# Kernel tuning notes

Measured on AMD Instinct MI355X. Metric: run time of the kernel, lower is better.

## Reference

```python
import jax, jax.numpy as jnp
import numpy as np

P_DROP = 0.1
NTYPES = 8
DROP_KEY = jax.random.key(42)


def _dropout(h, i):
    # deterministic training-mode dropout, mask fixed by layer index
    keep = jax.random.bernoulli(jax.random.fold_in(DROP_KEY, i), 1.0 - P_DROP, h.shape)
    return jnp.where(keep, h / (1.0 - P_DROP), 0.0).astype(h.dtype)


def _func_conv(h, src, dst, types, convW, convb, act):
    # gather src features along edges, mean-aggregate onto dst nodes,
    # then apply a per-gate-type linear transform.
    n_out = types.shape[0]
    msg = h[src]                                                  # [E, d]
    agg = jax.ops.segment_sum(msg, dst, num_segments=n_out)       # [n_out, d]
    deg = jax.ops.segment_sum(jnp.ones((src.shape[0],), h.dtype), dst,
                              num_segments=n_out)
    agg = agg / jnp.maximum(deg, 1.0)[:, None]
    out = jnp.zeros((n_out, convW.shape[2]), h.dtype)
    for t in range(convW.shape[0]):                                # ntypes is small & fixed
        mask = (types == t).astype(h.dtype)[:, None]
        out = out + (agg * mask) @ convW[t]
    out = out + convb[types]
    return jax.nn.relu(out) if act else out


def setup_inputs() -> dict:
    key = jax.random.key(0)
    ks = jax.random.split(key, 16)
    N0, N1, N2, N3 = 400_000, 200_000, 100_000, 50_000
    E0, E1, E2 = 1_600_000, 800_000, 400_000
    d, dout = 128, 64
    inp = {
        "features": jax.random.normal(ks[0], (N0, d), jnp.float32),
        "src0": jax.random.randint(ks[1], (E0,), 0, N0),
        "dst0": jax.random.randint(ks[2], (E0,), 0, N1),
        "types1": jax.random.randint(ks[3], (N1,), 0, NTYPES),
        "src1": jax.random.randint(ks[4], (E1,), 0, N1),
        "dst1": jax.random.randint(ks[5], (E1,), 0, N2),
        "types2": jax.random.randint(ks[6], (N2,), 0, NTYPES),
        "src2": jax.random.randint(ks[7], (E2,), 0, N2),
        "dst2": jax.random.randint(ks[8], (E2,), 0, N3),
        "types3": jax.random.randint(ks[9], (N3,), 0, NTYPES),
        # learned params
        "convW": jax.random.normal(ks[10], (NTYPES, d, d), jnp.float32) / np.sqrt(d),
        "convb": jnp.zeros((NTYPES, d), jnp.float32),
        "fcW": jax.random.normal(ks[11], (d, dout), jnp.float32) / np.sqrt(d),
        "fcb": jnp.zeros((dout,), jnp.float32),
    }
    return inp


def reference(features, src0, dst0, types1, src1, dst1, types2,
              src2, dst2, types3, convW, convb, fcW, fcb):
    blocks = [(src0, dst0, types1), (src1, dst1, types2), (src2, dst2, types3)]
    depth = len(blocks)
    h = features
    for i, (s, dst, t) in enumerate(blocks):
        if i != 0:
            h = _dropout(h, i)
        h = _func_conv(h, s, dst, t, convW, convb, act=(i != depth - 1))
    h = h @ fcW + fcb   # hidden_dim != out_dim -> fc_out applied
    return h            # squeeze(1) is a no-op for out_dim > 1
```

## Files before the change

### kernel.cpp

```cpp
#include <hip/hip_runtime.h>
#include <cstdint>
#include <cstddef>

__host__ __device__ inline void tf2x32(uint32_t k0, uint32_t k1,
                                       uint32_t x0, uint32_t x1,
                                       uint32_t* o0, uint32_t* o1)
{
    uint32_t ks2 = k0 ^ k1 ^ 0x1BD11BDAu;
    x0 += k0; x1 += k1;
#define TF_R(r) do { x0 += x1; x1 = (x1 << (r)) | (x1 >> (32 - (r))); x1 ^= x0; } while (0)
    TF_R(13); TF_R(15); TF_R(26); TF_R(6);
    x0 += k1;  x1 += ks2 + 1u;
    TF_R(17); TF_R(29); TF_R(16); TF_R(24);
    x0 += ks2; x1 += k0 + 2u;
    TF_R(13); TF_R(15); TF_R(26); TF_R(6);
    x0 += k0;  x1 += k1 + 3u;
    TF_R(17); TF_R(29); TF_R(16); TF_R(24);
    x0 += k1;  x1 += ks2 + 4u;
    TF_R(13); TF_R(15); TF_R(26); TF_R(6);
    x0 += ks2; x1 += k0 + 5u;
#undef TF_R
    *o0 = x0; *o1 = x1;
}

__device__ inline float drop_scale(uint32_t fk0, uint32_t fk1, uint32_t idx)
{
    uint32_t o0, o1;
    tf2x32(fk0, fk1, 0u, idx, &o0, &o1);
    uint32_t bits = o0 ^ o1;
    float u = __uint_as_float((bits >> 9) | 0x3f800000u) - 1.0f;
    return (u < 0.9f) ? (1.0f / 0.9f) : 0.0f;
}

__device__ inline ushort bf16_rn(float f)
{
    uint32_t u = __float_as_uint(f);
    u += 0x7fffu + ((u >> 16) & 1u);
    return (ushort)(u >> 16);
}
__device__ inline float bf16_f(ushort h) { return __uint_as_float(((uint32_t)h) << 16); }
__device__ inline uint32_t pack2bf(float a, float b)
{
    return (uint32_t)bf16_rn(a) | ((uint32_t)bf16_rn(b) << 16);
}
__device__ inline float bflo(uint32_t u) { return __uint_as_float(u << 16); }
__device__ inline float bfhi(uint32_t u) { return __uint_as_float(u & 0xffff0000u); }

typedef __attribute__((ext_vector_type(8))) short bf16x8;
typedef __attribute__((ext_vector_type(4))) float f32x4;

__global__ __launch_bounds__(256) void fcvt_kernel(
    const float4* __restrict__ in, uint2* __restrict__ out, long long n4)
{
    long long stride = (long long)gridDim.x * 256;
    for (long long i = blockIdx.x * 256LL + threadIdx.x; i < n4; i += stride) {
        float4 v = in[i];
        out[i] = make_uint2(pack2bf(v.x, v.y), pack2bf(v.z, v.w));
    }
}

__global__ __launch_bounds__(256) void prep_all_kernel(
    const float* __restrict__ convW, const float* __restrict__ convb,
    const float* __restrict__ fcW, const float* __restrict__ fcb,
    ushort* __restrict__ WThi, ushort* __restrict__ WTlo,
    ushort* __restrict__ WfThi, ushort* __restrict__ WfTlo,
    float* __restrict__ bfb)
{
    __shared__ float F[128 * 64];
    int t = blockIdx.x, tid = threadIdx.x;
    #pragma unroll
    for (int it = 0; it < 8; ++it) {
        int idx4 = (it * 256 + tid) * 4;
        *(float4*)&F[idx4] = *(const float4*)&fcW[idx4];
    }
    __syncthreads();

    {
        const float* S = convW + (size_t)t * 16384;
        ushort* DH = WThi + (size_t)t * 16384;
        ushort* DL = WTlo + (size_t)t * 16384;
        for (int idx = tid; idx < 16384; idx += 256) {
            int k = idx >> 7, c = idx & 127;
            float v = S[idx];
            ushort hi = bf16_rn(v);
            ushort lo = bf16_rn(v - bf16_f(hi));
            int pos = c * 128 + ((((k >> 3) ^ (c & 15)) << 3) | (k & 7));
            DH[pos] = hi; DL[pos] = lo;
        }
    }

    {
        int r = tid >> 1, cb = (tid & 1) * 32;
        const float* Wrow = convW + (size_t)t * 16384 + (size_t)r * 128;
        float acc[32];
        #pragma unroll
        for (int c = 0; c < 32; ++c) acc[c] = 0.f;
        for (int k = 0; k < 128; ++k) {
            float w = Wrow[k];
            #pragma unroll
            for (int c = 0; c < 32; ++c) acc[c] += w * F[k * 64 + cb + c];
        }
        ushort* FH = WfThi + (size_t)t * 8192;
        ushort* FL = WfTlo + (size_t)t * 8192;
        int swzr = (r & 7);
        #pragma unroll
        for (int c = 0; c < 32; ++c) {
            int col = cb + c;
            float v = acc[c];
            ushort hi = bf16_rn(v);
            ushort lo = bf16_rn(v - bf16_f(hi));
            int pos = col * 128 + ((((r >> 3) ^ (col & 15)) << 3) | swzr);
            FH[pos] = hi; FL[pos] = lo;
        }
    }

    if (tid < 64) {
        float a = fcb[tid];
        const float* bt = convb + (size_t)t * 128;
        for (int k = 0; k < 128; ++k) a += bt[k] * F[k * 64 + tid];
        bfb[(size_t)t * 64 + tid] = a;
    }
}

#define EPB 4096

__global__ __launch_bounds__(256) void hist_all_kernel(
    const int* __restrict__ d0, const int* __restrict__ d1, const int* __restrict__ d2,
    const int* __restrict__ t1, const int* __restrict__ t2, const int* __restrict__ t3,
    int E0, int E1, int E2, int N1, int N2, int N3,
    int nb0, int nb1, int nb2, int nblk0, int nblk1, int nblk2,
    uint32_t* __restrict__ tot, uint32_t* __restrict__ tcnt)
{
    int L = blockIdx.y;
    int tid = threadIdx.x;
    if (L < 3) {
        const int* dst = L == 0 ? d0 : (L == 1 ? d1 : d2);
        int E  = L == 0 ? E0 : (L == 1 ? E1 : E2);
        int NB = L == 0 ? nb0 : (L == 1 ? nb1 : nb2);
        int nblk = L == 0 ? nblk0 : (L == 1 ? nblk1 : nblk2);
        int gO = L == 0 ? 0 : (L == 1 ? nb0 : nb0 + nb1);
        if ((int)blockIdx.x >= nblk) return;
        __shared__ uint32_t lh[256];
        lh[tid] = 0;
        __syncthreads();
        int base = blockIdx.x * EPB;
        for (int i = tid; i < EPB; i += 256) {
            int e = base + i;
            if (e < E) atomicAdd(&lh[((uint32_t)dst[e]) >> 10], 1u);
        }
        __syncthreads();
        if (tid < NB && lh[tid]) atomicAdd(&tot[gO + tid], lh[tid]);
    } else {
        int totalN = N1 + N2 + N3;
        if ((int)blockIdx.x * 256 >= totalN) return;
        __shared__ uint32_t lh[24];
        if (tid < 24) lh[tid] = 0;
        __syncthreads();
        int i = blockIdx.x * 256 + tid;
        if (i < N1) atomicAdd(&lh[t1[i]], 1u);
        else if (i < N1 + N2) atomicAdd(&lh[8 + t2[i - N1]], 1u);
        else if (i < totalN) atomicAdd(&lh[16 + t3[i - N1 - N2]], 1u);
        __syncthreads();
        if (tid < 24 && lh[tid]) atomicAdd(&tcnt[tid], lh[tid]);
    }
}

__global__ __launch_bounds__(512) void scan_all_kernel(
    const uint32_t* __restrict__ tot, uint32_t* __restrict__ bo,
    uint32_t* __restrict__ bcur, uint32_t* __restrict__ rowptr3,
    const uint32_t* __restrict__ tcnt, int* __restrict__ boff,
    uint32_t* __restrict__ tcur, int* __restrict__ order3,
    int nb0, int nb1, int nb2, int N1, int N2, int N3,
    int r1, int r2, int no1p, int no2p)
{
    __shared__ uint32_t bol[348];
    __shared__ int pB[27];
    __shared__ int cnts[24];
    int t = threadIdx.x;
    int TB = nb0 + nb1 + nb2;
    if (t < 3) {
        int nb = t == 0 ? nb0 : (t == 1 ? nb1 : nb2);
        int g0 = t == 0 ? 0 : (t == 1 ? nb0 : nb0 + nb1);
        int gi0 = g0 + t;
        uint32_t run = 0;
        for (int i = 0; i < nb; ++i) { bol[gi0 + i] = run; run += tot[g0 + i]; }
        bol[gi0 + nb] = run;
        int rp = t == 0 ? 0 : (t == 1 ? r1 : r2);
        int N = t == 0 ? N1 : (t == 1 ? N2 : N3);
        rowptr3[rp + N] = run;
    }
    if (t == 3) {
        for (int L = 0; L < 3; ++L) {
            int a = 0;
            for (int ty = 0; ty < 8; ++ty) {
                pB[L * 9 + ty] = a;
                int c = (int)tcnt[L * 8 + ty];
                cnts[L * 8 + ty] = c;
                tcur[L * 8 + ty] = (uint32_t)a;
                a += (c + 127) & ~127;
            }
            pB[L * 9 + 8] = a;
        }
    }
    __syncthreads();
    for (int i = t; i < TB + 3; i += 512) bo[i] = bol[i];
    if (t < TB) {
        int layer = t < nb0 ? 0 : (t < nb0 + nb1 ? 1 : 2);
        bcur[t] = bol[t + layer];
    }
    if (t < 27) boff[t] = pB[t];
    if (t < 24) {
        int L = t >> 3, ty = t & 7;
        int noff = L == 0 ? 0 : (L == 1 ? no1p : no2p);
        int s = pB[L * 9 + ty] + cnts[t];
        int e2 = pB[L * 9 + ty + 1];
        for (int k = s; k < e2; ++k) order3[noff + k] = -1;
    }
}

__global__ __launch_bounds__(256) void scatter_all_kernel(
    const int* __restrict__ s0, const int* __restrict__ d0,
    const int* __restrict__ s1, const int* __restrict__ d1,
    const int* __restrict__ s2, const int* __restrict__ d2,
    const int* __restrict__ t1, const int* __restrict__ t2, const int* __restrict__ t3,
    int E0, int E1, int E2, int N1, int N2, int N3,
    int nb0, int nb1, int nb2, int nblk0, int nblk1, int nblk2,
    uint32_t* __restrict__ bcur, uint32_t* __restrict__ pairs,
    uint32_t* __restrict__ tcur, int* __restrict__ order3, int no1p, int no2p)
{
    int L = blockIdx.y;
    int tid = threadIdx.x;
    if (L < 3) {
        const int* src = L == 0 ? s0 : (L == 1 ? s1 : s2);
        const int* dst = L == 0 ? d0 : (L == 1 ? d1 : d2);
        int E  = L == 0 ? E0 : (L == 1 ? E1 : E2);
        int NB = L == 0 ? nb0 : (L == 1 ? nb1 : nb2);
        int nblk = L == 0 ? nblk0 : (L == 1 ? nblk1 : nblk2);
        int gO = L == 0 ? 0 : (L == 1 ? nb0 : nb0 + nb1);
        uint32_t* pr = pairs + (L == 0 ? 0 : (L == 1 ? E0 : E0 + E1));
        if ((int)blockIdx.x >= nblk) return;

        __shared__ uint32_t lh[256], lbase[256], rank[256];
        lh[tid] = 0; rank[tid] = 0;
        __syncthreads();
        int base = blockIdx.x * EPB;
        for (int i = tid; i < EPB; i += 256) {
            int e = base + i;
            if (e < E) atomicAdd(&lh[((uint32_t)dst[e]) >> 10], 1u);
        }
        __syncthreads();
        if (tid < NB && lh[tid]) lbase[tid] = atomicAdd(&bcur[gO + tid], lh[tid]);
        __syncthreads();
        for (int i = tid; i < EPB; i += 256) {
            int e = base + i;
            if (e < E) {
                uint32_t d = (uint32_t)dst[e];
                uint32_t bk = d >> 10;
                uint32_t r = atomicAdd(&rank[bk], 1u);
                pr[lbase[bk] + r] = ((d & 1023u) << 22) | (uint32_t)src[e];
            }
        }
    } else {
        int totalN = N1 + N2 + N3;
        if ((int)blockIdx.x * 256 >= totalN) return;
        __shared__ uint32_t lh[24], lbase[24];
        if (tid < 24) lh[tid] = 0;
        __syncthreads();
        int i = blockIdx.x * 256 + tid;
        int slot = -1, idx = 0; uint32_t r = 0;
        if (i < N1) { idx = i; slot = t1[idx]; }
        else if (i < N1 + N2) { idx = i - N1; slot = 8 + t2[idx]; }
        else if (i < totalN) { idx = i - N1 - N2; slot = 16 + t3[idx]; }
        if (slot >= 0) r = atomicAdd(&lh[slot], 1u);
        __syncthreads();
        if (tid < 24 && lh[tid]) lbase[tid] = atomicAdd(&tcur[tid], lh[tid]);
        __syncthreads();
        if (slot >= 0) {
            int noff = slot < 8 ? 0 : (slot < 16 ? no1p : no2p);
            order3[noff + lbase[slot] + r] = idx;
        }
    }
}

__global__ __launch_bounds__(256) void bfill_kernel(
    const uint32_t* __restrict__ bo, const uint32_t* __restrict__ pairs,
    int* __restrict__ elist3, uint32_t* __restrict__ rowptr3,
    int nb0, int nb1, int nb2, int N1, int N2, int N3,
    int E0, int E1, int r1, int r2)
{
    __shared__ uint32_t hist[1024];
    __shared__ uint32_t cur[1024];
    __shared__ uint32_t psum[256];
    int g = blockIdx.x, tid = threadIdx.x;
    int layer, lb, N, Eoff, rp;
    if (g < nb0) { layer = 0; lb = g; N = N1; Eoff = 0; rp = 0; }
    else if (g < nb0 + nb1) { layer = 1; lb = g - nb0; N = N2; Eoff = E0; rp = r1; }
    else { layer = 2; lb = g - nb0 - nb1; N = N3; Eoff = E0 + E1; rp = r2; }
    uint32_t off = bo[g + layer], end = bo[g + layer + 1];
    int nodeBase = lb << 10;
    int nodesIn = N - nodeBase; if (nodesIn > 1024) nodesIn = 1024;

    #pragma unroll
    for (int i = 0; i < 4; ++i) hist[tid * 4 + i] = 0;
    __syncthreads();
    for (uint32_t e = off + tid; e < end; e += 256)
        atomicAdd(&hist[pairs[Eoff + e] >> 22], 1u);
    __syncthreads();

    uint32_t x[4]; uint32_t s = 0;
    #pragma unroll
    for (int i = 0; i < 4; ++i) { x[i] = hist[tid * 4 + i]; s += x[i]; }
    psum[tid] = s; __syncthreads();
    uint32_t inc = s;
    #pragma unroll
    for (int o = 1; o < 256; o <<= 1) {
        uint32_t y = (tid >= o) ? psum[tid - o] : 0u;
        __syncthreads();
        inc += y; psum[tid] = inc;
        __syncthreads();
    }
    uint32_t run = off + inc - s;
    #pragma unroll
    for (int i = 0; i < 4; ++i) { cur[tid * 4 + i] = run; run += x[i]; }
    __syncthreads();

    for (int i = tid; i < nodesIn; i += 256)
        rowptr3[rp + nodeBase + i] = cur[i];
    __syncthreads();

    for (uint32_t e = off + tid; e < end; e += 256) {
        uint32_t pk = pairs[Eoff + e];
        uint32_t pos = atomicAdd(&cur[pk >> 22], 1u);
        elist3[Eoff + pos] = (int)(pk & 0x3FFFFFu);
    }
}

__global__ __launch_bounds__(256) void aggregate_kernel(
    const uint32_t* __restrict__ hbf, const uint32_t* __restrict__ rowptr,
    const int* __restrict__ elist, uint32_t* __restrict__ agghi,
    uint32_t* __restrict__ agglo, int nout)
{
    int wid = threadIdx.x >> 6, lane = threadIdx.x & 63;
    int n0 = blockIdx.x * 8 + wid * 2;
    if (n0 >= nout) return;
    int n1 = n0 + 1;
    bool v1 = (n1 < nout);
    uint32_t b0 = rowptr[n0], e0 = rowptr[n0 + 1];
    uint32_t b1 = v1 ? rowptr[n1] : 0u, e1 = v1 ? rowptr[n1 + 1] : 0u;
    const uint32_t* base = hbf + lane;
    float a0x = 0.f, a0y = 0.f, a1x = 0.f, a1y = 0.f;
    uint32_t i0 = b0, i1 = b1;

    if (i0 + 8 <= e0 && i1 + 8 <= e1) {
        int ia[8], ib[8];
        #pragma unroll
        for (int k = 0; k < 8; ++k) { ia[k] = elist[i0 + k]; ib[k] = elist[i1 + k]; }
        for (;;) {
            uint32_t u[8], w[8];
            #pragma unroll
            for (int k = 0; k < 8; ++k) u[k] = base[(size_t)ia[k] * 64];
            #pragma unroll
            for (int k = 0; k < 8; ++k) w[k] = base[(size_t)ib[k] * 64];
            i0 += 8; i1 += 8;
            bool more = (i0 + 8 <= e0 && i1 + 8 <= e1);
            if (more) {
                #pragma unroll
                for (int k = 0; k < 8; ++k) { ia[k] = elist[i0 + k]; ib[k] = elist[i1 + k]; }
            }
            #pragma unroll
            for (int k = 0; k < 8; ++k) { a0x += bflo(u[k]); a0y += bfhi(u[k]); }
            #pragma unroll
            for (int k = 0; k < 8; ++k) { a1x += bflo(w[k]); a1y += bfhi(w[k]); }
            if (!more) break;
        }
    }
    while (i0 + 4 <= e0 && i1 + 4 <= e1) {
        uint32_t u[4], w[4];
        #pragma unroll
        for (int k = 0; k < 4; ++k) u[k] = base[(size_t)elist[i0 + k] * 64];
        #pragma unroll
        for (int k = 0; k < 4; ++k) w[k] = base[(size_t)elist[i1 + k] * 64];
        #pragma unroll
        for (int k = 0; k < 4; ++k) { a0x += bflo(u[k]); a0y += bfhi(u[k]); }
        #pragma unroll
        for (int k = 0; k < 4; ++k) { a1x += bflo(w[k]); a1y += bfhi(w[k]); }
        i0 += 4; i1 += 4;
    }
    while (i0 + 4 <= e0) {
        uint32_t u[4];
        #pragma unroll
        for (int k = 0; k < 4; ++k) u[k] = base[(size_t)elist[i0 + k] * 64];
        #pragma unroll
        for (int k = 0; k < 4; ++k) { a0x += bflo(u[k]); a0y += bfhi(u[k]); }
        i0 += 4;
    }
    while (i1 + 4 <= e1) {
        uint32_t w[4];
        #pragma unroll
        for (int k = 0; k < 4; ++k) w[k] = base[(size_t)elist[i1 + k] * 64];
        #pragma unroll
        for (int k = 0; k < 4; ++k) { a1x += bflo(w[k]); a1y += bfhi(w[k]); }
        i1 += 4;
    }
    for (; i0 < e0; ++i0) {
        uint32_t u = base[(size_t)elist[i0] * 64];
        a0x += bflo(u); a0y += bfhi(u);
    }
    for (; i1 < e1; ++i1) {
        uint32_t w = base[(size_t)elist[i1] * 64];
        a1x += bflo(w); a1y += bfhi(w);
    }

    float sc0 = 1.0f / fmaxf((float)(e0 - b0), 1.0f);
    a0x *= sc0; a0y *= sc0;
    ushort hx = bf16_rn(a0x); ushort lx = bf16_rn(a0x - bf16_f(hx));
    ushort hy = bf16_rn(a0y); ushort ly = bf16_rn(a0y - bf16_f(hy));
    agghi[(size_t)n0 * 64 + lane] = (uint32_t)hx | ((uint32_t)hy << 16);
    agglo[(size_t)n0 * 64 + lane] = (uint32_t)lx | ((uint32_t)ly << 16);
    if (v1) {
        float sc1 = 1.0f / fmaxf((float)(e1 - b1), 1.0f);
        a1x *= sc1; a1y *= sc1;
        ushort hx1 = bf16_rn(a1x); ushort lx1 = bf16_rn(a1x - bf16_f(hx1));
        ushort hy1 = bf16_rn(a1y); ushort ly1 = bf16_rn(a1y - bf16_f(hy1));
        agghi[(size_t)n1 * 64 + lane] = (uint32_t)hx1 | ((uint32_t)hy1 << 16);
        agglo[(size_t)n1 * 64 + lane] = (uint32_t)lx1 | ((uint32_t)ly1 << 16);
    }
}

template<int DOUT, bool RELU, bool DROP, bool OUTBF>
__global__ __launch_bounds__(512) void mfma_gemm_kernel(
    const uint32_t* __restrict__ agghi, const uint32_t* __restrict__ agglo,
    const int* __restrict__ order, const int* __restrict__ off,
    const ushort* __restrict__ WThi, const ushort* __restrict__ WTlo,
    const float* __restrict__ bias8, void* __restrict__ houtv,
    uint32_t fk0, uint32_t fk1)
{
    __shared__ ushort WH[DOUT * 128];
    __shared__ ushort WL[DOUT * 128];
    __shared__ int ND[128];

    int b0 = blockIdx.x * 128;
    if (b0 >= off[8]) return;
    int t = 0;
    #pragma unroll
    for (int u = 1; u < 8; ++u) if (b0 >= off[u]) ++t;
    int tid = threadIdx.x;

    if (tid < 128) ND[tid] = order[b0 + tid];

    {
        const float4* sh = (const float4*)(WThi + (size_t)t * DOUT * 128);
        const float4* sl = (const float4*)(WTlo + (size_t)t * DOUT * 128);
        float4* dh = (float4*)WH; float4* dl = (float4*)WL;
        #pragma unroll
        for (int it = 0; it < DOUT * 16 / 512; ++it) {
            int c = it * 512 + tid;
            dh[c] = sh[c]; dl[c] = sl[c];
        }
    }
    __syncthreads();

    int wid = tid >> 6, lane = tid & 63;
    int r15 = lane & 15, q = lane >> 4;
    int arow = wid * 16 + r15;
    int nd_a = ND[arow];

    const bf16x8* gh = (const bf16x8*)agghi;
    const bf16x8* gl = (const bf16x8*)agglo;
    bf16x8 zero8 = (bf16x8){0, 0, 0, 0, 0, 0, 0, 0};
    bf16x8 ahv[4], alv[4];
    {
        size_t rowb = (size_t)(nd_a < 0 ? 0 : nd_a) * 16;
        #pragma unroll
        for (int ks = 0; ks < 4; ++ks) {
            size_t ix = rowb + (q + ks * 4);
            ahv[ks] = (nd_a >= 0) ? gh[ix] : zero8;
            alv[ks] = (nd_a >= 0) ? gl[ix] : zero8;
        }
    }

    constexpr int NF = DOUT / 16;
    f32x4 acc[NF];
    #pragma unroll
    for (int i = 0; i < NF; ++i) acc[i] = (f32x4){0.f, 0.f, 0.f, 0.f};

    const bf16x8* WHp = (const bf16x8*)WH;
    const bf16x8* WLp = (const bf16x8*)WL;

    #pragma unroll
    for (int ks = 0; ks < 4; ++ks) {
        int sch = (q + ks * 4) ^ r15;
        bf16x8 ah = ahv[ks];
        bf16x8 al = alv[ks];
        #pragma unroll
        for (int nf = 0; nf < NF; ++nf) {
            int col = nf * 16 + r15;
            bf16x8 bh = WHp[col * 16 + sch];
            bf16x8 bl = WLp[col * 16 + sch];
            acc[nf] = __builtin_amdgcn_mfma_f32_16x16x32_bf16(ah, bh, acc[nf], 0, 0, 0);
            acc[nf] = __builtin_amdgcn_mfma_f32_16x16x32_bf16(ah, bl, acc[nf], 0, 0, 0);
            acc[nf] = __builtin_amdgcn_mfma_f32_16x16x32_bf16(al, bh, acc[nf], 0, 0, 0);
        }
    }

    int ndr[4];
    #pragma unroll
    for (int r = 0; r < 4; ++r) ndr[r] = ND[wid * 16 + q * 4 + r];
    const float* bptr = bias8 + (size_t)t * DOUT;

    #pragma unroll
    for (int nf = 0; nf < NF; ++nf) {
        int col = nf * 16 + r15;
        float bv = bptr[col];
        float vr[4];
        #pragma unroll
        for (int r = 0; r < 4; ++r) {
            float v = acc[nf][r] + bv;
            if (RELU) v = fmaxf(v, 0.f);
            if (DROP) {
                int nd = ndr[r] < 0 ? 0 : ndr[r];
                v *= drop_scale(fk0, fk1, (uint32_t)nd * 128u + (uint32_t)col);
            }
            vr[r] = v;
        }
        if (OUTBF) {
            uint32_t* hb = (uint32_t*)houtv;
            #pragma unroll
            for (int r = 0; r < 4; ++r) {
                float w = __shfl_xor(vr[r], 1, 64);
                if ((lane & 1) == 0 && ndr[r] >= 0)
                    hb[(size_t)ndr[r] * (DOUT / 2) + (col >> 1)] = pack2bf(vr[r], w);
            }
        } else {
            float* ho = (float*)houtv;
            #pragma unroll
            for (int r = 0; r < 4; ++r)
                if (ndr[r] >= 0) ho[(size_t)ndr[r] * DOUT + col] = vr[r];
        }
    }
}

extern "C" void kernel_launch(void* const* d_in, const int* in_sizes, int n_in,
                              void* d_out, int out_size, void* d_ws, size_t ws_size,
                              hipStream_t stream)
{
    const float* features = (const float*)d_in[0];
    const int*   src0 = (const int*)d_in[1];
    const int*   dst0 = (const int*)d_in[2];
    const int*   types1 = (const int*)d_in[3];
    const int*   src1 = (const int*)d_in[4];
    const int*   dst1 = (const int*)d_in[5];
    const int*   types2 = (const int*)d_in[6];
    const int*   src2 = (const int*)d_in[7];
    const int*   dst2 = (const int*)d_in[8];
    const int*   types3 = (const int*)d_in[9];
    const float* convW = (const float*)d_in[10];
    const float* convb = (const float*)d_in[11];
    const float* fcW   = (const float*)d_in[12];
    const float* fcb   = (const float*)d_in[13];

    int N0 = in_sizes[0] / 128;
    int E0 = in_sizes[1], N1 = in_sizes[3];
    int E1 = in_sizes[4], N2 = in_sizes[6];
    int E2 = in_sizes[7], N3 = in_sizes[9];
    int totalN = N1 + N2 + N3;
    int totalE = E0 + E1 + E2;
    int r1 = N1 + 1, r2 = N1 + 1 + N2 + 1;
    int no1p = N1 + 1024, no2p = no1p + N2 + 1024;
    int maxN = N1 > N2 ? N1 : N2; if (N3 > maxN) maxN = N3;

    int nb0 = (N1 + 1023) >> 10, nb1 = (N2 + 1023) >> 10, nb2 = (N3 + 1023) >> 10;
    int TB = nb0 + nb1 + nb2;
    int nblk0 = (E0 + EPB - 1) / EPB, nblk1 = (E1 + EPB - 1) / EPB, nblk2 = (E2 + EPB - 1) / EPB;
    int nblkMax = nblk0 > nblk1 ? nblk0 : nblk1; if (nblk2 > nblkMax) nblkMax = nblk2;
    int nblkT = (totalN + 255) / 256;
    int gx = nblkMax > nblkT ? nblkMax : nblkT;

    char* ws = (char*)d_ws;
    size_t woff = 0;
    auto alloc = [&](size_t bytes) -> void* {
        void* p = ws + woff;
        woff = (woff + bytes + 255) & ~(size_t)255;
        return p;
    };
    uint32_t* fbf     = (uint32_t*)alloc((size_t)N0 * 64 * 4);
    uint32_t* hbf     = fbf;
    uint32_t* aggHi   = (uint32_t*)alloc((size_t)maxN * 64 * 4);
    uint32_t* pairs   = aggHi;
    uint32_t* aggLo   = (uint32_t*)alloc((size_t)maxN * 64 * 4);
    uint32_t* rowptr3 = (uint32_t*)alloc((size_t)(totalN + 3) * 4);
    int*      elist3  = (int*)alloc((size_t)totalE * 4);
    int*      order3  = (int*)alloc((size_t)(totalN + 3 * 1024) * 4);
    uint32_t* tot     = (uint32_t*)alloc((size_t)(TB + 8 + 24) * 4);
    uint32_t* tcnt    = tot + TB + 8;
    uint32_t* bcur    = (uint32_t*)alloc((size_t)(TB + 8) * 4);
    uint32_t* bo      = (uint32_t*)alloc((size_t)(TB + 3) * 4);
    int*      boff    = (int*)alloc(27 * 4);
    uint32_t* tcur    = (uint32_t*)alloc(24 * 4);
    float*    bfb     = (float*)alloc((size_t)8 * 64 * 4);
    ushort*   WThi    = (ushort*)alloc((size_t)8 * 128 * 128 * 2);
    ushort*   WTlo    = (ushort*)alloc((size_t)8 * 128 * 128 * 2);
    ushort*   WfThi   = (ushort*)alloc((size_t)8 * 64 * 128 * 2);
    ushort*   WfTlo   = (ushort*)alloc((size_t)8 * 64 * 128 * 2);
    (void)ws_size; (void)n_in; (void)out_size;

    fcvt_kernel<<<4096, 256, 0, stream>>>(
        (const float4*)features, (uint2*)fbf, (long long)N0 * 32);
    prep_all_kernel<<<8, 256, 0, stream>>>(
        convW, convb, fcW, fcb, WThi, WTlo, WfThi, WfTlo, bfb);

    hipMemsetAsync(tot, 0, (size_t)(TB + 8 + 24) * 4, stream);
    hist_all_kernel<<<dim3(gx, 4), 256, 0, stream>>>(
        dst0, dst1, dst2, types1, types2, types3,
        E0, E1, E2, N1, N2, N3, nb0, nb1, nb2, nblk0, nblk1, nblk2, tot, tcnt);
    scan_all_kernel<<<1, 512, 0, stream>>>(
        tot, bo, bcur, rowptr3, tcnt, boff, tcur, order3,
        nb0, nb1, nb2, N1, N2, N3, r1, r2, no1p, no2p);
    scatter_all_kernel<<<dim3(gx, 4), 256, 0, stream>>>(
        src0, dst0, src1, dst1, src2, dst2, types1, types2, types3,
        E0, E1, E2, N1, N2, N3, nb0, nb1, nb2, nblk0, nblk1, nblk2,
        bcur, pairs, tcur, order3, no1p, no2p);
    bfill_kernel<<<TB, 256, 0, stream>>>(bo, pairs, elist3, rowptr3,
        nb0, nb1, nb2, N1, N2, N3, E0, E1, r1, r2);

    uint32_t fk1a, fk1b, fk2a, fk2b;
    tf2x32(0u, 42u, 0u, 1u, &fk1a, &fk1b);
    tf2x32(0u, 42u, 0u, 2u, &fk2a, &fk2b);

    aggregate_kernel<<<(N1 + 7) / 8, 256, 0, stream>>>(
        fbf, rowptr3, elist3, aggHi, aggLo, N1);
    mfma_gemm_kernel<128, true, true, true><<<(N1 + 127) / 128 + 8, 512, 0, stream>>>(
        aggHi, aggLo, order3, boff, WThi, WTlo, convb, hbf, fk1a, fk1b);

    aggregate_kernel<<<(N2 + 7) / 8, 256, 0, stream>>>(
        hbf, rowptr3 + r1, elist3 + E0, aggHi, aggLo, N2);
    mfma_gemm_kernel<128, true, true, true><<<(N2 + 127) / 128 + 8, 512, 0, stream>>>(
        aggHi, aggLo, order3 + no1p, boff + 9, WThi, WTlo, convb, hbf, fk2a, fk2b);

    aggregate_kernel<<<(N3 + 7) / 8, 256, 0, stream>>>(
        hbf, rowptr3 + r2, elist3 + E0 + E1, aggHi, aggLo, N3);
    mfma_gemm_kernel<64, false, false, false><<<(N3 + 127) / 128 + 8, 512, 0, stream>>>(
        aggHi, aggLo, order3 + no2p, boff + 18, WfThi, WfTlo, bfb, d_out, 0u, 0u);
}
```

Before: 581.9 us.

## Reuse per-block bucket histograms in scatter and simplify aggregate gather loop

The histogram kernel now stores each block's per-bucket counts to a workspace array. The scatter kernel reads those counts back instead of recomputing the local histogram, which removes one pass over the dst indices and its shared-memory atomics. Separately, the aggregate kernel drops its software-pipelined index prefetch in favour of a plain loop that loads indices and gathers rows in the same iteration. That leaves more scheduling to the compiler and may expose more gather latency.

```diff
diff --git a/kernel.cpp b/kernel.cpp
--- a/kernel.cpp
+++ b/kernel.cpp
@@ -129,7 +129,9 @@
     const int* __restrict__ t1, const int* __restrict__ t2, const int* __restrict__ t3,
     int E0, int E1, int E2, int N1, int N2, int N3,
     int nb0, int nb1, int nb2, int nblk0, int nblk1, int nblk2,
-    uint32_t* __restrict__ tot, uint32_t* __restrict__ tcnt)
+    int cO0, int cO1, int cO2,
+    uint32_t* __restrict__ tot, uint32_t* __restrict__ tcnt,
+    uint32_t* __restrict__ cnt)
 {
     int L = blockIdx.y;
     int tid = threadIdx.x;
@@ -139,6 +141,7 @@
         int NB = L == 0 ? nb0 : (L == 1 ? nb1 : nb2);
         int nblk = L == 0 ? nblk0 : (L == 1 ? nblk1 : nblk2);
         int gO = L == 0 ? 0 : (L == 1 ? nb0 : nb0 + nb1);
+        int cO = L == 0 ? cO0 : (L == 1 ? cO1 : cO2);
         if ((int)blockIdx.x >= nblk) return;
         __shared__ uint32_t lh[256];
         lh[tid] = 0;
@@ -149,7 +152,10 @@
             if (e < E) atomicAdd(&lh[((uint32_t)dst[e]) >> 10], 1u);
         }
         __syncthreads();
-        if (tid < NB && lh[tid]) atomicAdd(&tot[gO + tid], lh[tid]);
+        if (tid < NB) {
+            cnt[cO + (size_t)blockIdx.x * NB + tid] = lh[tid];
+            if (lh[tid]) atomicAdd(&tot[gO + tid], lh[tid]);
+        }
     } else {
         int totalN = N1 + N2 + N3;
         if ((int)blockIdx.x * 256 >= totalN) return;
@@ -225,6 +231,7 @@
     const int* __restrict__ t1, const int* __restrict__ t2, const int* __restrict__ t3,
     int E0, int E1, int E2, int N1, int N2, int N3,
     int nb0, int nb1, int nb2, int nblk0, int nblk1, int nblk2,
+    int cO0, int cO1, int cO2, const uint32_t* __restrict__ cnt,
     uint32_t* __restrict__ bcur, uint32_t* __restrict__ pairs,
     uint32_t* __restrict__ tcur, int* __restrict__ order3, int no1p, int no2p)
 {
@@ -237,20 +244,19 @@
         int NB = L == 0 ? nb0 : (L == 1 ? nb1 : nb2);
         int nblk = L == 0 ? nblk0 : (L == 1 ? nblk1 : nblk2);
         int gO = L == 0 ? 0 : (L == 1 ? nb0 : nb0 + nb1);
+        int cO = L == 0 ? cO0 : (L == 1 ? cO1 : cO2);
         uint32_t* pr = pairs + (L == 0 ? 0 : (L == 1 ? E0 : E0 + E1));
         if ((int)blockIdx.x >= nblk) return;
 
-        __shared__ uint32_t lh[256], lbase[256], rank[256];
-        lh[tid] = 0; rank[tid] = 0;
+        __shared__ uint32_t lbase[256], rank[256];
+        rank[tid] = 0;
+        __syncthreads();
+        if (tid < NB) {
+            uint32_t c = cnt[cO + (size_t)blockIdx.x * NB + tid];
+            if (c) lbase[tid] = atomicAdd(&bcur[gO + tid], c);
+        }
         __syncthreads();
         int base = blockIdx.x * EPB;
-        for (int i = tid; i < EPB; i += 256) {
-            int e = base + i;
-            if (e < E) atomicAdd(&lh[((uint32_t)dst[e]) >> 10], 1u);
-        }
-        __syncthreads();
-        if (tid < NB && lh[tid]) lbase[tid] = atomicAdd(&bcur[gO + tid], lh[tid]);
-        __syncthreads();
         for (int i = tid; i < EPB; i += 256) {
             int e = base + i;
             if (e < E) {
@@ -351,28 +357,17 @@
     float a0x = 0.f, a0y = 0.f, a1x = 0.f, a1y = 0.f;
     uint32_t i0 = b0, i1 = b1;
 
-    if (i0 + 8 <= e0 && i1 + 8 <= e1) {
-        int ia[8], ib[8];
-        #pragma unroll
-        for (int k = 0; k < 8; ++k) { ia[k] = elist[i0 + k]; ib[k] = elist[i1 + k]; }
-        for (;;) {
-            uint32_t u[8], w[8];
-            #pragma unroll
-            for (int k = 0; k < 8; ++k) u[k] = base[(size_t)ia[k] * 64];
-            #pragma unroll
-            for (int k = 0; k < 8; ++k) w[k] = base[(size_t)ib[k] * 64];
-            i0 += 8; i1 += 8;
-            bool more = (i0 + 8 <= e0 && i1 + 8 <= e1);
-            if (more) {
-                #pragma unroll
-                for (int k = 0; k < 8; ++k) { ia[k] = elist[i0 + k]; ib[k] = elist[i1 + k]; }
-            }
-            #pragma unroll
-            for (int k = 0; k < 8; ++k) { a0x += bflo(u[k]); a0y += bfhi(u[k]); }
-            #pragma unroll
-            for (int k = 0; k < 8; ++k) { a1x += bflo(w[k]); a1y += bfhi(w[k]); }
-            if (!more) break;
-        }
+    while (i0 + 8 <= e0 && i1 + 8 <= e1) {
+        uint32_t u[8], w[8];
+        #pragma unroll
+        for (int k = 0; k < 8; ++k) u[k] = base[(size_t)elist[i0 + k] * 64];
+        #pragma unroll
+        for (int k = 0; k < 8; ++k) w[k] = base[(size_t)elist[i1 + k] * 64];
+        #pragma unroll
+        for (int k = 0; k < 8; ++k) { a0x += bflo(u[k]); a0y += bfhi(u[k]); }
+        #pragma unroll
+        for (int k = 0; k < 8; ++k) { a1x += bflo(w[k]); a1y += bfhi(w[k]); }
+        i0 += 8; i1 += 8;
     }
     while (i0 + 4 <= e0 && i1 + 4 <= e1) {
         uint32_t u[4], w[4];
@@ -575,6 +570,10 @@
     int nblkMax = nblk0 > nblk1 ? nblk0 : nblk1; if (nblk2 > nblkMax) nblkMax = nblk2;
     int nblkT = (totalN + 255) / 256;
     int gx = nblkMax > nblkT ? nblkMax : nblkT;
+    int cO0 = 0;
+    int cO1 = cO0 + nblk0 * nb0;
+    int cO2 = cO1 + nblk1 * nb1;
+    int cntEntries = cO2 + nblk2 * nb2;
 
     char* ws = (char*)d_ws;
     size_t woff = 0;
@@ -591,6 +590,7 @@
     uint32_t* rowptr3 = (uint32_t*)alloc((size_t)(totalN + 3) * 4);
     int*      elist3  = (int*)alloc((size_t)totalE * 4);
     int*      order3  = (int*)alloc((size_t)(totalN + 3 * 1024) * 4);
+    uint32_t* cnt     = (uint32_t*)alloc((size_t)cntEntries * 4);
     uint32_t* tot     = (uint32_t*)alloc((size_t)(TB + 8 + 24) * 4);
     uint32_t* tcnt    = tot + TB + 8;
     uint32_t* bcur    = (uint32_t*)alloc((size_t)(TB + 8) * 4);
@@ -612,14 +612,15 @@
     hipMemsetAsync(tot, 0, (size_t)(TB + 8 + 24) * 4, stream);
     hist_all_kernel<<<dim3(gx, 4), 256, 0, stream>>>(
         dst0, dst1, dst2, types1, types2, types3,
-        E0, E1, E2, N1, N2, N3, nb0, nb1, nb2, nblk0, nblk1, nblk2, tot, tcnt);
+        E0, E1, E2, N1, N2, N3, nb0, nb1, nb2, nblk0, nblk1, nblk2,
+        cO0, cO1, cO2, tot, tcnt, cnt);
     scan_all_kernel<<<1, 512, 0, stream>>>(
         tot, bo, bcur, rowptr3, tcnt, boff, tcur, order3,
         nb0, nb1, nb2, N1, N2, N3, r1, r2, no1p, no2p);
     scatter_all_kernel<<<dim3(gx, 4), 256, 0, stream>>>(
         src0, dst0, src1, dst1, src2, dst2, types1, types2, types3,
         E0, E1, E2, N1, N2, N3, nb0, nb1, nb2, nblk0, nblk1, nblk2,
-        bcur, pairs, tcur, order3, no1p, no2p);
+        cO0, cO1, cO2, cnt, bcur, pairs, tcur, order3, no1p, no2p);
     bfill_kernel<<<TB, 256, 0, stream>>>(bo, pairs, elist3, rowptr3,
         nb0, nb1, nb2, N1, N2, N3, E0, E1, r1, r2);
 
```

After: 538.5 us. 7.5% less time.
